# Kernel tuning notes

Hardware: AMD Instinct MI355X
Metric: run time of the kernel (lower is better)

## Reference

```python
import jax, jax.numpy as jnp
import numpy as np

EPS_NORM = 1e-12
BN_EPS = 1e-5

def rmsnorm(x, gamma):
    # F.normalize(x, dim=-1) * gamma * dim**0.5
    n = jnp.maximum(jnp.linalg.norm(x, axis=-1, keepdims=True), EPS_NORM)
    return x / n * gamma * np.float32(np.sqrt(x.shape[-1]))

def conv1d(x, w, pad):
    # x: (B,C,T), w: (O,I,K)
    return jax.lax.conv_general_dilated(x, w, (1,), [(pad, pad)],
                                        dimension_numbers=('NCH', 'OIH', 'NCH'))

def maxpool3(x):
    # kernel 3, stride 1, pad 1 over last axis
    return jax.lax.reduce_window(x, -jnp.inf, jax.lax.max,
                                 (1, 1, 3), (1, 1, 1), [(0, 0), (0, 0), (1, 1)])

def gelu(x):
    return jax.nn.gelu(x, approximate=False)  # matches torch F.gelu default


def setup_inputs() -> dict:
    key = jax.random.key(0)
    ks = jax.random.split(key, 16)
    B, N, D, E, H, NF = 4, 4096, 512, 4, 1024, 32
    s = 0.02
    inp = {
        'x': jax.random.normal(ks[0], (B, N, D), jnp.float32),
        'left_k': 2048,
        'gamma1': jnp.ones((D,), jnp.float32),
        'gamma2': jnp.ones((D,), jnp.float32),
        'attn_w': jax.random.normal(ks[1], (D, 1), jnp.float32) * s,
        'attn_b': jnp.zeros((1,), jnp.float32),
        'gate_w': jax.random.normal(ks[2], (D, E), jnp.float32) * s,
        'expert_w1': jax.random.normal(ks[3], (E, D, H), jnp.float32) * s,
        'expert_w2': jax.random.normal(ks[4], (E, H, D), jnp.float32) * s,
        'bott_w': jax.random.normal(ks[5], (NF, D, 1), jnp.float32) * s,
        'conv_w39': jax.random.normal(ks[6], (NF, NF, 39), jnp.float32) * s,
        'conv_w19': jax.random.normal(ks[7], (NF, NF, 19), jnp.float32) * s,
        'conv_w9': jax.random.normal(ks[8], (NF, NF, 9), jnp.float32) * s,
        'mp_w': jax.random.normal(ks[9], (NF, D, 1), jnp.float32) * s,
        'bn_g': jnp.ones((NF * 4,), jnp.float32),
        'bn_b': jnp.zeros((NF * 4,), jnp.float32),
        'proj_w': jax.random.normal(ks[10], (NF * 4, D), jnp.float32) * s,
        'proj_b': jnp.zeros((D,), jnp.float32),
    }
    return inp


def reference(x, left_k, gamma1, gamma2, attn_w, attn_b, gate_w,
              expert_w1, expert_w2, bott_w, conv_w39, conv_w19, conv_w9,
              mp_w, bn_g, bn_b, proj_w, proj_b):
    B, N, D = x.shape
    E = gate_w.shape[-1]

    x_n = rmsnorm(x, gamma1)
    scores = jax.nn.sigmoid(x_n @ attn_w + attn_b)            # (B,N,1)
    xs = x_n * scores                                          # (B,N,D)

    # top-k token selection (remain_ratio < 1 path)
    _, top_idx = jax.lax.top_k(scores[..., 0], left_k)         # (B,left_k)
    sorted_idx = jnp.sort(top_idx, axis=1)
    left_x = jnp.take_along_axis(xs, sorted_idx[..., None], axis=1)
    # complement sum via scatter mask (faithful to scatter_/gather/sum)
    sel = jnp.zeros((B, N), x.dtype).at[jnp.arange(B)[:, None], sorted_idx].set(1.0)
    extra = jnp.einsum('bn,bnd->bd', 1.0 - sel, xs)[:, None, :]
    xcat = jnp.concatenate([left_x, extra], axis=1)            # (B,left_k+1,D)

    x_n2 = rmsnorm(xcat, gamma2)

    # dense soft MoE
    gate = jax.nn.softmax(x_n2 @ gate_w, axis=-1)              # (B,T,E)
    h = gelu(jnp.einsum('btd,edh->bteh', x_n2, expert_w1))
    eo = jnp.einsum('bteh,ehd->bted', h, expert_w2)
    moe_out = jnp.einsum('bte,bted->btd', gate, eo)
    moe_loss = E * jnp.sum(jnp.mean(gate, axis=(0, 1)) ** 2)

    # Inception branch (channels-first)
    xc = jnp.transpose(x_n2, (0, 2, 1))                        # (B,D,T)
    xb = conv1d(xc, bott_w, 0)                                 # (B,32,T)
    outs = [conv1d(xb, conv_w39, 19), conv1d(xb, conv_w19, 9),
            conv1d(xb, conv_w9, 4), conv1d(maxpool3(xc), mp_w, 0)]
    cat = jnp.concatenate(outs, axis=1)                        # (B,128,T)
    mu = jnp.mean(cat, axis=(0, 2), keepdims=True)
    var = jnp.var(cat, axis=(0, 2), keepdims=True)
    bn = (cat - mu) / jnp.sqrt(var + BN_EPS) * bn_g[None, :, None] + bn_b[None, :, None]
    incep = gelu(bn)
    incep_out = jnp.transpose(incep, (0, 2, 1)) @ proj_w + proj_b  # (B,T,D)

    out = xcat + moe_out + incep_out
    return gelu(out), moe_loss
```

## Files before the change

### kernel.cpp

```cpp
#include <hip/hip_runtime.h>
#include <hip/hip_bf16.h>
#include <math.h>

#define DEV __device__ __forceinline__

constexpr int B_ = 4, N_ = 4096, D_ = 512, E_ = 4, H_ = 1024, NF_ = 32;
constexpr int KL_ = 2048, T_ = KL_ + 1;
constexpr int TOK_ = B_ * T_;
constexpr int SP_ = 2304;

typedef __bf16 bf16x8 __attribute__((ext_vector_type(8)));
typedef float f32x4 __attribute__((ext_vector_type(4)));

DEV float gelu_f(float x){
  float t = __expf(-1.702f * x);
  return x * __builtin_amdgcn_rcpf(1.0f + t);
}
DEV float bf2f(unsigned short u){ union{unsigned int i; float f;} c; c.i = (unsigned)u << 16; return c.f; }
DEV unsigned pack2(float a, float b){
  __hip_bfloat16 ha = __float2bfloat16(a), hb = __float2bfloat16(b);
  unsigned short ua = *(unsigned short*)&ha, ub = *(unsigned short*)&hb;
  return (unsigned)ua | ((unsigned)ub << 16);
}

DEV float wave_sum(float v){
  #pragma unroll
  for (int off = 32; off > 0; off >>= 1) v += __shfl_down(v, off, 64);
  return v;
}

DEV float block_sum256(float v, float* sm){
  v = wave_sum(v);
  int lane = threadIdx.x & 63, wid = threadIdx.x >> 6;
  if (lane == 0) sm[wid] = v;
  __syncthreads();
  if (threadIdx.x == 0) sm[0] = sm[0] + sm[1] + sm[2] + sm[3];
  __syncthreads();
  float r = sm[0];
  __syncthreads();
  return r;
}

__global__ void k_rms_score(const float* __restrict__ x, const float* __restrict__ g,
                            const float* __restrict__ aw, const float* __restrict__ ab,
                            float* __restrict__ scores, float* __restrict__ scale){
  __shared__ float sm[4];
  int row = blockIdx.x; int tid = threadIdx.x;
  const float* xr = x + (size_t)row * D_;
  float v0 = xr[tid], v1 = xr[tid + 256];
  float ss = block_sum256(v0 * v0 + v1 * v1, sm);
  float a  = block_sum256(v0 * g[tid] * aw[tid] + v1 * g[tid + 256] * aw[tid + 256], sm);
  float n = fmaxf(sqrtf(ss), 1e-12f);
  float inv = 22.627416997969522f / n;
  float z = inv * a + ab[0];
  float s = 1.0f / (1.0f + expf(-z));
  if (tid == 0){ scores[row] = s; scale[row] = inv * s; }
}

__global__ void k_select(const float* __restrict__ scores, int* __restrict__ flags){
  __shared__ float s[N_];
  __shared__ int cnts[4][64];
  int b = blockIdx.y; int tid = threadIdx.x;
  int tile = blockIdx.x * 64;
  const float4* src = (const float4*)(scores + (size_t)b * N_);
  for (int j = tid; j < N_ / 4; j += 256) ((float4*)s)[j] = src[j];
  __syncthreads();
  int tok = tid & 63, part = tid >> 6;
  int i = tile + tok;
  float si = s[i];
  int cnt = 0;
  const float4* sp = (const float4*)(s + part * 1024);
  int jb = part * 1024;
  #pragma unroll 4
  for (int j = 0; j < 256; j++){
    float4 v = sp[j];
    int j4 = jb + j * 4;
    cnt += (v.x > si) || (v.x == si && (j4 + 0) < i);
    cnt += (v.y > si) || (v.y == si && (j4 + 1) < i);
    cnt += (v.z > si) || (v.z == si && (j4 + 2) < i);
    cnt += (v.w > si) || (v.w == si && (j4 + 3) < i);
  }
  cnts[part][tok] = cnt;
  __syncthreads();
  if (tid < 64){
    int c = cnts[0][tid] + cnts[1][tid] + cnts[2][tid] + cnts[3][tid];
    flags[(size_t)b * N_ + tile + tid] = (c < KL_) ? 1 : 0;
  }
}

__global__ void k_compact(const int* __restrict__ flags, int* __restrict__ idx){
  __shared__ int wsum[4];
  int b = blockIdx.x; int tid = threadIdx.x;
  const int* fb = flags + (size_t)b * N_;
  int f[16]; int cnt = 0;
  #pragma unroll
  for (int i = 0; i < 16; i++){ f[i] = fb[tid * 16 + i]; cnt += f[i]; }
  int lane = tid & 63, wid = tid >> 6;
  int v = cnt;
  #pragma unroll
  for (int off = 1; off < 64; off <<= 1){
    int t = __shfl_up(v, off, 64);
    if (lane >= off) v += t;
  }
  if (lane == 63) wsum[wid] = v;
  __syncthreads();
  int base = v - cnt;
  for (int w = 0; w < wid; w++) base += wsum[w];
  int* ib = idx + (size_t)b * KL_;
  #pragma unroll
  for (int i = 0; i < 16; i++){
    if (f[i]) ib[base++] = tid * 16 + i;
  }
}

DEV void rms2_tail(int row, float xc0, float xc1,
                   const float* __restrict__ g2, const float* __restrict__ gw,
                   __hip_bfloat16* __restrict__ xcatb,
                   __hip_bfloat16* __restrict__ xn2b, float* __restrict__ gate,
                   float* sm, float* sg){
  int tid = threadIdx.x;
  __hip_bfloat16* xb = xcatb + (size_t)row * D_;
  xb[tid] = __float2bfloat16(xc0); xb[tid + 256] = __float2bfloat16(xc1);
  float ss = block_sum256(xc0 * xc0 + xc1 * xc1, sm);
  float n = fmaxf(sqrtf(ss), 1e-12f);
  float inv = 22.627416997969522f / n;
  float xn0 = xc0 * inv * g2[tid], xn1 = xc1 * inv * g2[tid + 256];
  __hip_bfloat16* ob = xn2b + (size_t)row * D_;
  ob[tid] = __float2bfloat16(xn0); ob[tid + 256] = __float2bfloat16(xn1);
  const float4* gw4 = (const float4*)gw;
  float4 wa = gw4[tid], wb = gw4[tid + 256];
  float l0 = xn0 * wa.x + xn1 * wb.x, l1 = xn0 * wa.y + xn1 * wb.y;
  float l2 = xn0 * wa.z + xn1 * wb.z, l3 = xn0 * wa.w + xn1 * wb.w;
  l0 = wave_sum(l0); l1 = wave_sum(l1); l2 = wave_sum(l2); l3 = wave_sum(l3);
  int lane = tid & 63, wid = tid >> 6;
  if (lane == 0){ sg[wid*4+0]=l0; sg[wid*4+1]=l1; sg[wid*4+2]=l2; sg[wid*4+3]=l3; }
  __syncthreads();
  if (tid == 0){
    float a0 = sg[0]+sg[4]+sg[8]+sg[12];
    float a1 = sg[1]+sg[5]+sg[9]+sg[13];
    float a2 = sg[2]+sg[6]+sg[10]+sg[14];
    float a3 = sg[3]+sg[7]+sg[11]+sg[15];
    float m = fmaxf(fmaxf(a0, a1), fmaxf(a2, a3));
    float e0 = expf(a0-m), e1 = expf(a1-m), e2 = expf(a2-m), e3 = expf(a3-m);
    float is = 1.f / (e0+e1+e2+e3);
    float* gr = gate + (size_t)row * 4;
    gr[0]=e0*is; gr[1]=e1*is; gr[2]=e2*is; gr[3]=e3*is;
  }
}

__global__ void k_gatherrms(const float* __restrict__ x, const float* __restrict__ scale,
                            const float* __restrict__ g1, const float* __restrict__ g2,
                            const float* __restrict__ gw, const int* __restrict__ idx,
                            __hip_bfloat16* __restrict__ xcatb,
                            __hip_bfloat16* __restrict__ xn2b, float* __restrict__ gate){
  __shared__ float sm[4];
  __shared__ float sg[16];
  int rid = blockIdx.x;
  int b = rid >> 11, p = rid & (KL_ - 1);
  int tid = threadIdx.x;
  int tok = idx[(size_t)b * KL_ + p];
  float sc = scale[(size_t)b * N_ + tok];
  const float* xr = x + ((size_t)b * N_ + tok) * D_;
  float xc0 = xr[tid] * sc * g1[tid];
  float xc1 = xr[tid + 256] * sc * g1[tid + 256];
  rms2_tail(b * T_ + p, xc0, xc1, g2, gw, xcatb, xn2b, gate, sm, sg);
}

__global__ void k_extra1(const float* __restrict__ x, const float* __restrict__ scale,
                         const int* __restrict__ flags, float* __restrict__ part){
  int b = blockIdx.y, blk = blockIdx.x;
  int tid = threadIdx.x;
  const int* fb = flags + (size_t)b * N_ + blk * 64;
  const float* sb = scale + (size_t)b * N_ + blk * 64;
  const float2* xp = (const float2*)(x + ((size_t)b * N_ + blk * 64) * D_) + tid;
  float2 acc = {0.f, 0.f};
  for (int i = 0; i < 64; i++){
    if (!fb[i]){
      float s = sb[i];
      float2 v = xp[(size_t)i * 256];
      acc.x += v.x * s; acc.y += v.y * s;
    }
  }
  float* pr = part + ((size_t)(b * 64 + blk)) * D_;
  pr[tid * 2] = acc.x; pr[tid * 2 + 1] = acc.y;
}

__global__ void k_extra2r(const float* __restrict__ part, const float* __restrict__ g1,
                          const float* __restrict__ g2, const float* __restrict__ gw,
                          __hip_bfloat16* __restrict__ xcatb,
                          __hip_bfloat16* __restrict__ xn2b, float* __restrict__ gate){
  __shared__ float sm[4];
  __shared__ float sg[16];
  int b = blockIdx.x; int tid = threadIdx.x;
  float s0 = 0.f, s1 = 0.f;
  for (int i = 0; i < 64; i++){
    const float* pr = part + ((size_t)(b * 64 + i)) * D_;
    s0 += pr[tid]; s1 += pr[tid + 256];
  }
  float xc0 = s0 * g1[tid], xc1 = s1 * g1[tid + 256];
  rms2_tail(b * T_ + KL_, xc0, xc1, g2, gw, xcatb, xn2b, gate, sm, sg);
}

__global__ void k_gsumloss(const float* __restrict__ gate, float* __restrict__ o){
  __shared__ float sm[16];
  int tid = threadIdx.x;
  float4 a = {0.f, 0.f, 0.f, 0.f};
  for (int r = tid; r < TOK_; r += 256){
    float4 v = *(const float4*)(gate + (size_t)r * 4);
    a.x += v.x; a.y += v.y; a.z += v.z; a.w += v.w;
  }
  a.x = wave_sum(a.x); a.y = wave_sum(a.y); a.z = wave_sum(a.z); a.w = wave_sum(a.w);
  int lane = tid & 63, wid = tid >> 6;
  if (lane == 0){ sm[wid*4]=a.x; sm[wid*4+1]=a.y; sm[wid*4+2]=a.z; sm[wid*4+3]=a.w; }
  __syncthreads();
  if (tid == 0){
    float l = 0.f;
    #pragma unroll
    for (int e = 0; e < 4; e++){
      float s = sm[e] + sm[4+e] + sm[8+e] + sm[12+e];
      float m = s / (float)TOK_;
      l += m * m;
    }
    o[0] = (float)E_ * l;
  }
}

DEV void trb_tile(const float* __restrict__ in, __hip_bfloat16* __restrict__ out,
                  int R, int C, int bx, int by){
  __shared__ float t[32][33];
  int c0 = bx * 32, r0 = by * 32;
  int j = threadIdx.x & 31, i4 = threadIdx.x >> 5;
  #pragma unroll
  for (int k = 0; k < 4; k++){
    int i = i4 * 4 + k;
    t[i][j] = in[(size_t)(r0 + i) * C + c0 + j];
  }
  __syncthreads();
  #pragma unroll
  for (int k = 0; k < 4; k++){
    int i = i4 * 4 + k;
    out[(size_t)(c0 + i) * R + r0 + j] = __float2bfloat16(t[j][i]);
  }
}

__global__ void k_wprep(const float* __restrict__ ew1, const float* __restrict__ ew2,
                        const float* __restrict__ proj_w,
                        const float* __restrict__ w39, const float* __restrict__ w19,
                        const float* __restrict__ w9,
                        __hip_bfloat16* __restrict__ w1b, __hip_bfloat16* __restrict__ w2b,
                        __hip_bfloat16* __restrict__ projb, __hip_bfloat16* __restrict__ wcb,
                        float* __restrict__ stats){
  int blk = blockIdx.x;
  int tid = threadIdx.x;
  if (blk < 2048){
    int e = blk >> 9, rem = blk & 511;
    int by = rem >> 5, bx = rem & 31;
    trb_tile(ew1 + (size_t)e * D_ * H_, w1b + (size_t)e * D_ * H_, D_, H_, bx, by);
  } else if (blk < 4096){
    int r = blk - 2048;
    int e = r >> 9, r2 = r & 511;
    int bx = r2 & 15, by = r2 >> 4;
    __shared__ float t[32][33];
    const float* ip = ew2 + (size_t)e * H_ * D_;
    __hip_bfloat16* op = w2b + (size_t)e * H_;
    int c0 = bx * 32, r0 = by * 32;
    int j = tid & 31, i4 = tid >> 5;
    #pragma unroll
    for (int k = 0; k < 4; k++){
      int i = i4 * 4 + k;
      t[i][j] = ip[(size_t)(r0 + i) * D_ + c0 + j];
    }
    __syncthreads();
    #pragma unroll
    for (int k = 0; k < 4; k++){
      int i = i4 * 4 + k;
      int v = r0 + j;
      int pv = (v & ~63) | ((v & 15) << 2) | ((v >> 4) & 3);
      op[(size_t)(c0 + i) * 4096 + pv] = __float2bfloat16(t[j][i]);
    }
  } else if (blk < 4160){
    int r = blk - 4096;
    trb_tile(proj_w, projb, 128, D_, r & 15, r >> 4);
  } else if (blk < 4448){
    int i = (blk - 4160) * 256 + tid;
    if (i < 73728){
      const float* w; int KP, KW, base;
      if (i < 40960){ w = w39; KP = 40; KW = 39; base = 0; }
      else if (i < 61440){ w = w19; KP = 20; KW = 19; base = 40960; }
      else { w = w9; KP = 12; KW = 9; base = 61440; }
      int li = i - base;
      int oc = li / (32 * KP);
      int rem = li % (32 * KP);
      int k = rem >> 5, ic = rem & 31;
      float v = (k < KW) ? w[((size_t)oc * 32 + ic) * KW + k] : 0.f;
      wcb[i] = __float2bfloat16(v);
    }
  } else {
    stats[tid] = 0.f;
  }
}

template<int EPI>
__launch_bounds__(512)
__global__ void gemm_bt(const __hip_bfloat16* __restrict__ A,
                        const __hip_bfloat16* __restrict__ Bt,
                        __hip_bfloat16* __restrict__ Cb, size_t zstride,
                        int M, int N, int K, int kloc,
                        const float* __restrict__ gatep){
  __shared__ __align__(16) char smem[2][24576];
  int tid = threadIdx.x;
  unsigned gx = gridDim.x;
  unsigned nwg = gx * gridDim.y;
  unsigned orig = blockIdx.x + gx * blockIdx.y;
  unsigned q = nwg >> 3, r = nwg & 7;
  unsigned xcd = orig & 7, loc = orig >> 3;
  unsigned wg = (xcd < r ? xcd * (q + 1) : r * (q + 1) + (xcd - r) * q) + loc;
  int m0 = (int)(wg / gx) * 256, n0 = (int)(wg % gx) * 128;
  int z = blockIdx.z;
  int koff = z * kloc;
  int ln = tid & 63, wid = tid >> 6;
  int wm = wid >> 1, wn = wid & 1;

  f32x4 acc[4][4] = {};

  auto stage = [&](int buf, int k0){
    #pragma unroll
    for (int c = 0; c < 2; c++){
      int ii = tid + c * 512;
      int rr = ii >> 2, s = ii & 3;
      int gm = m0 + rr; gm = gm < M ? gm : M - 1;
      const __hip_bfloat16* gp = A + (size_t)gm * K + (koff + k0 + ((s ^ (rr & 3)) << 3));
      __builtin_amdgcn_global_load_lds(
          (const __attribute__((address_space(1))) void*)gp,
          (__attribute__((address_space(3))) void*)&smem[buf][ii * 16], 16, 0, 0);
    }
    {
      int ii = tid;
      int rr = ii >> 2, s = ii & 3;
      const __hip_bfloat16* gp = Bt + (size_t)(n0 + rr) * K + (koff + k0 + ((s ^ (rr & 3)) << 3));
      __builtin_amdgcn_global_load_lds(
          (const __attribute__((address_space(1))) void*)gp,
          (__attribute__((address_space(3))) void*)&smem[buf][16384 + ii * 16], 16, 0, 0);
    }
  };

  int nk = kloc >> 5;
  stage(0, 0);
  __syncthreads();
  int slotb = (((ln >> 4) ^ (ln & 3)) << 4);
  for (int t = 0; t < nk; t++){
    int buf = t & 1;
    if (t + 1 < nk) stage(buf ^ 1, (t + 1) << 5);
    bf16x8 af[4], bfr[4];
    #pragma unroll
    for (int m = 0; m < 4; m++){
      int R = wm * 64 + m * 16 + (ln & 15);
      af[m] = *(const bf16x8*)&smem[buf][R * 64 + slotb];
    }
    #pragma unroll
    for (int n = 0; n < 4; n++){
      int R = wn * 64 + n * 16 + (ln & 15);
      bfr[n] = *(const bf16x8*)&smem[buf][16384 + R * 64 + slotb];
    }
    #pragma unroll
    for (int m = 0; m < 4; m++)
      #pragma unroll
      for (int n = 0; n < 4; n++)
        acc[m][n] = __builtin_amdgcn_mfma_f32_16x16x32_bf16(af[m], bfr[n], acc[m][n], 0, 0, 0);
    __syncthreads();
  }

  __hip_bfloat16* Co = Cb + (size_t)z * zstride;
  int e = n0 >> 10;
  int lr = ln & 15;
  #pragma unroll
  for (int m = 0; m < 4; m++){
    int rb = m0 + wm * 64 + m * 16 + ((ln >> 4) << 2);
    float gv[4];
    if (EPI == 1){
      #pragma unroll
      for (int r2 = 0; r2 < 4; r2++)
        gv[r2] = (rb + r2 < M) ? gatep[(size_t)(rb + r2) * 4 + e] : 0.f;
    }
    #pragma unroll
    for (int r2 = 0; r2 < 4; r2++){
      int row = rb + r2;
      if (row < M){
        float v0 = acc[m][0][r2], v1 = acc[m][1][r2];
        float v2 = acc[m][2][r2], v3 = acc[m][3][r2];
        if (EPI == 1){
          v0 = gelu_f(v0) * gv[r2]; v1 = gelu_f(v1) * gv[r2];
          v2 = gelu_f(v2) * gv[r2]; v3 = gelu_f(v3) * gv[r2];
        }
        uint2 pk; pk.x = pack2(v0, v1); pk.y = pack2(v2, v3);
        size_t ci = (size_t)row * N + (n0 + wn * 64 + 4 * lr);
        *(uint2*)&Co[ci] = pk;
      }
    }
  }
}

__global__ void k_1x1F(const __hip_bfloat16* __restrict__ xn2b, const float* __restrict__ bw,
                       const float* __restrict__ mw,
                       __hip_bfloat16* __restrict__ xbp, float* __restrict__ cat,
                       float* __restrict__ stats){
  __shared__ float Xs[32 * 33];
  __shared__ float Ws[32 * 36];
  int type = blockIdx.y;
  const float* w = type == 0 ? bw : mw;
  int tid = threadIdx.x;
  int G0 = blockIdx.x * 32;
  int tok = tid & 31, grp = tid >> 5;
  float acc[4] = {};
  for (int d0 = 0; d0 < D_; d0 += 32){
    {
      int tt = tid >> 3, dc = (tid & 7) * 4;
      int g = G0 + tt;
      float4 v = {0.f, 0.f, 0.f, 0.f};
      if (g < TOK_){
        const __hip_bfloat16* p = xn2b + (size_t)g * D_ + d0 + dc;
        ushort4 rw = *(const ushort4*)p;
        v.x = bf2f(rw.x); v.y = bf2f(rw.y); v.z = bf2f(rw.z); v.w = bf2f(rw.w);
        if (type == 1){
          int t = g % T_;
          if (t > 0){
            ushort4 u = *(const ushort4*)(p - D_);
            v.x = fmaxf(v.x, bf2f(u.x)); v.y = fmaxf(v.y, bf2f(u.y));
            v.z = fmaxf(v.z, bf2f(u.z)); v.w = fmaxf(v.w, bf2f(u.w));
          }
          if (t < T_ - 1){
            ushort4 u = *(const ushort4*)(p + D_);
            v.x = fmaxf(v.x, bf2f(u.x)); v.y = fmaxf(v.y, bf2f(u.y));
            v.z = fmaxf(v.z, bf2f(u.z)); v.w = fmaxf(v.w, bf2f(u.w));
          }
        }
      }
      float* xd = &Xs[tt * 33 + dc];
      xd[0] = v.x; xd[1] = v.y; xd[2] = v.z; xd[3] = v.w;
    }
    for (int j = tid; j < 1024; j += 256){
      int f = j >> 5, d = j & 31;
      Ws[d * 36 + f] = w[(size_t)f * D_ + d0 + d];
    }
    __syncthreads();
    const float* xr = &Xs[tok * 33];
    #pragma unroll 8
    for (int d = 0; d < 32; d++){
      float xv = xr[d];
      const float4* w4 = (const float4*)&Ws[d * 36 + grp * 4];
      float4 a = w4[0];
      acc[0] += xv * a.x; acc[1] += xv * a.y; acc[2] += xv * a.z; acc[3] += xv * a.w;
    }
    __syncthreads();
  }
  int g = G0 + tok;
  bool valid = g < TOK_;
  if (valid){
    if (type == 0){
      int bb = g / T_, t = g % T_;
      __hip_bfloat16* op = xbp + ((size_t)(bb * SP_ + 32 + t)) * 32 + grp * 4;
      #pragma unroll
      for (int j = 0; j < 4; j++) op[j] = __float2bfloat16(acc[j]);
    } else {
      float* op = cat + (size_t)g * 128 + 96 + grp * 4;
      #pragma unroll
      for (int j = 0; j < 4; j++) op[j] = acc[j];
    }
  }
  if (type == 1){
    #pragma unroll
    for (int j = 0; j < 4; j++){
      float s = valid ? acc[j] : 0.f;
      float qv = valid ? acc[j] * acc[j] : 0.f;
      #pragma unroll
      for (int off = 16; off > 0; off >>= 1){
        s += __shfl_down(s, off, 32);
        qv += __shfl_down(qv, off, 32);
      }
      if (tok == 0){
        int ch = 96 + grp * 4 + j;
        atomicAdd(&stats[ch], s);
        atomicAdd(&stats[128 + ch], qv);
      }
    }
  }
}

template<int KP, int PAD, int OFF, int TYPE>
DEV void convm_body(const __hip_bfloat16* __restrict__ xbp,
                    const __hip_bfloat16* __restrict__ wcb,
                    float* __restrict__ cat, float* __restrict__ stats,
                    char* smem, float* bsS, float* bsQ){
  constexpr int R = KP * 32;
  int t0 = blockIdx.x * 128, b = blockIdx.y;
  int tid = threadIdx.x;
  if (tid < 32){ bsS[tid] = 0.f; bsQ[tid] = 0.f; }
  for (int j = tid; j < 768; j += 256){
    int r = j >> 2, c = j & 3;
    int rg = b * SP_ + 32 + t0 - PAD + r;
    const __hip_bfloat16* gp = xbp + (size_t)rg * 32 + ((c ^ (r & 3)) << 3);
    __builtin_amdgcn_global_load_lds(
        (const __attribute__((address_space(1))) void*)gp,
        (__attribute__((address_space(3))) void*)(smem + j * 16), 16, 0, 0);
  }
  __syncthreads();
  int ln = tid & 63, wid = tid >> 6;
  int lr = ln & 15, lg = ln >> 4;
  int tb = wid * 32;
  const __hip_bfloat16* wt = wcb + OFF;
  const __hip_bfloat16* bp0 = wt + (size_t)lr * R + lg * 8;
  const __hip_bfloat16* bp1 = wt + (size_t)(16 + lr) * R + lg * 8;
  f32x4 acc[2][2] = {};
  bf16x8 bc0 = *(const bf16x8*)bp0;
  bf16x8 bc1 = *(const bf16x8*)bp1;
  #pragma unroll 4
  for (int s = 0; s < KP; s++){
    bf16x8 bn0 = bc0, bn1 = bc1;
    if (s + 1 < KP){
      bn0 = *(const bf16x8*)(bp0 + (s + 1) * 32);
      bn1 = *(const bf16x8*)(bp1 + (s + 1) * 32);
    }
    int ra0 = tb + lr + s;
    int ra1 = tb + 16 + lr + s;
    bf16x8 a0 = *(const bf16x8*)(smem + ra0 * 64 + ((lg ^ (ra0 & 3)) << 4));
    bf16x8 a1 = *(const bf16x8*)(smem + ra1 * 64 + ((lg ^ (ra1 & 3)) << 4));
    acc[0][0] = __builtin_amdgcn_mfma_f32_16x16x32_bf16(a0, bc0, acc[0][0], 0, 0, 0);
    acc[0][1] = __builtin_amdgcn_mfma_f32_16x16x32_bf16(a0, bc1, acc[0][1], 0, 0, 0);
    acc[1][0] = __builtin_amdgcn_mfma_f32_16x16x32_bf16(a1, bc0, acc[1][0], 0, 0, 0);
    acc[1][1] = __builtin_amdgcn_mfma_f32_16x16x32_bf16(a1, bc1, acc[1][1], 0, 0, 0);
    bc0 = bn0; bc1 = bn1;
  }
  float sN[2] = {0.f, 0.f}, qN[2] = {0.f, 0.f};
  #pragma unroll
  for (int m = 0; m < 2; m++){
    int rb = tb + m * 16 + (lg << 2);
    #pragma unroll
    for (int n = 0; n < 2; n++){
      int oc = n * 16 + lr;
      #pragma unroll
      for (int j2 = 0; j2 < 4; j2++){
        int tp = t0 + rb + j2;
        if (tp < T_){
          float v = acc[m][n][j2];
          cat[((size_t)b * T_ + tp) * 128 + TYPE * 32 + oc] = v;
          sN[n] += v; qN[n] += v * v;
        }
      }
    }
  }
  #pragma unroll
  for (int n = 0; n < 2; n++){
    float s = sN[n], qv = qN[n];
    s += __shfl_down(s, 32, 64); qv += __shfl_down(qv, 32, 64);
    s += __shfl_down(s, 16, 64); qv += __shfl_down(qv, 16, 64);
    if (ln < 16){
      atomicAdd(&bsS[n * 16 + lr], s);
      atomicAdd(&bsQ[n * 16 + lr], qv);
    }
  }
  __syncthreads();
  if (tid < 32){
    atomicAdd(&stats[TYPE * 32 + tid], bsS[tid]);
    atomicAdd(&stats[128 + TYPE * 32 + tid], bsQ[tid]);
  }
}

__global__ __launch_bounds__(256)
void k_convM(const __hip_bfloat16* __restrict__ xbp,
             const __hip_bfloat16* __restrict__ wcb, float* __restrict__ cat,
             float* __restrict__ stats){
  __shared__ __align__(16) char smem[192 * 64];
  __shared__ float bsS[32], bsQ[32];
  if (blockIdx.z == 0)      convm_body<40, 19, 0,     0>(xbp, wcb, cat, stats, smem, bsS, bsQ);
  else if (blockIdx.z == 1) convm_body<20, 9,  40960, 1>(xbp, wcb, cat, stats, smem, bsS, bsQ);
  else                      convm_body<12, 4,  61440, 2>(xbp, wcb, cat, stats, smem, bsS, bsQ);
}

__global__ void k_bnact(const float* __restrict__ cat, __hip_bfloat16* __restrict__ catb,
                        const float* __restrict__ stats,
                        const float* __restrict__ g, const float* __restrict__ b){
  int i = blockIdx.x * 256 + threadIdx.x;
  int c = i & 127;
  float mu = stats[c] * (1.f / TOK_);
  float var = stats[128 + c] * (1.f / TOK_) - mu * mu;
  float v = cat[i];
  v = (v - mu) * rsqrtf(var + 1e-5f) * g[c] + b[c];
  catb[i] = __float2bfloat16(gelu_f(v));
}

__global__ void k_final(const __hip_bfloat16* __restrict__ xcatb,
                        const __hip_bfloat16* __restrict__ moeb,
                        size_t zs, const __hip_bfloat16* __restrict__ ioutb,
                        const float* __restrict__ pb, float* __restrict__ out){
  size_t i = ((size_t)blockIdx.x * 256 + threadIdx.x) * 2;
  int p = (int)(i & 511);
  size_t rowbase = i - p;
  float s0 = 0.f, s1 = 0.f;
  #pragma unroll
  for (int z = 0; z < 4; z++){
    unsigned u = *(const unsigned*)&moeb[(size_t)z * zs + i];
    s0 += bf2f((unsigned short)(u & 0xffff));
    s1 += bf2f((unsigned short)(u >> 16));
  }
  unsigned v = *(const unsigned*)&ioutb[i];
  s0 += bf2f((unsigned short)(v & 0xffff));
  s1 += bf2f((unsigned short)(v >> 16));
  int d0 = (p & ~63) | ((p & 3) << 4) | ((p >> 2) & 15);
  int p1 = p + 1;
  int d1 = (p1 & ~63) | ((p1 & 3) << 4) | ((p1 >> 2) & 15);
  const unsigned short* xc = (const unsigned short*)xcatb;
  s0 += bf2f(xc[rowbase + d0]) + pb[d0];
  s1 += bf2f(xc[rowbase + d1]) + pb[d1];
  out[rowbase + d0] = gelu_f(s0);
  out[rowbase + d1] = gelu_f(s1);
}

extern "C" void kernel_launch(void* const* d_in, const int* in_sizes, int n_in,
                              void* d_out, int out_size, void* d_ws, size_t ws_size,
                              hipStream_t stream){
  const float* x      = (const float*)d_in[0];
  const float* gamma1 = (const float*)d_in[2];
  const float* gamma2 = (const float*)d_in[3];
  const float* attn_w = (const float*)d_in[4];
  const float* attn_b = (const float*)d_in[5];
  const float* gate_w = (const float*)d_in[6];
  const float* ew1    = (const float*)d_in[7];
  const float* ew2    = (const float*)d_in[8];
  const float* bott_w = (const float*)d_in[9];
  const float* w39    = (const float*)d_in[10];
  const float* w19    = (const float*)d_in[11];
  const float* w9     = (const float*)d_in[12];
  const float* mp_w   = (const float*)d_in[13];
  const float* bn_g   = (const float*)d_in[14];
  const float* bn_b   = (const float*)d_in[15];
  const float* proj_w = (const float*)d_in[16];
  const float* proj_b = (const float*)d_in[17];
  float* out = (float*)d_out;

  float* ws = (float*)d_ws;
  size_t off = 0;
  auto alloc = [&](size_t n){ size_t o = off; off += (n + 63) & ~(size_t)63; return o; };
  size_t f_hb   = alloc((size_t)TOK_ * 4096 / 2);
  size_t f_sc   = alloc(B_ * N_);
  size_t f_sca  = alloc(B_ * N_);
  size_t f_fl   = alloc(B_ * N_);
  size_t f_idx  = alloc(B_ * KL_);
  size_t f_xcb  = alloc((size_t)TOK_ * D_ / 2 + 64);
  size_t f_moeb = alloc((size_t)4 * TOK_ * D_ / 2 + 64);
  size_t f_gate = alloc(TOK_ * E_);
  size_t f_st   = alloc(256);
  size_t f_xbp  = alloc((size_t)B_ * SP_ * 32 / 2);
  size_t f_cat  = alloc((size_t)TOK_ * 128);
  size_t f_wb   = alloc((size_t)(E_ * D_ * H_) + (size_t)TOK_ * D_ / 2 + 64);
  size_t f_part = alloc((size_t)B_ * 64 * D_);
  size_t f_wcb  = alloc(73728 / 2 + 64);
  size_t f_pjb  = alloc(512 * 128 / 2 + 64);
  (void)ws_size; (void)in_sizes; (void)n_in; (void)out_size;

  float* sc   = ws + f_sc;
  float* sca  = ws + f_sca;
  int*   fl   = (int*)(ws + f_fl);
  int*   idx  = (int*)(ws + f_idx);
  float* gate = ws + f_gate;
  float* stats= ws + f_st;
  float* cat  = ws + f_cat;
  float* part = ws + f_part;
  __hip_bfloat16* xcatb = (__hip_bfloat16*)(ws + f_xcb);
  __hip_bfloat16* moeb  = (__hip_bfloat16*)(ws + f_moeb);
  __hip_bfloat16* xbp   = (__hip_bfloat16*)(ws + f_xbp);
  __hip_bfloat16* wcb   = (__hip_bfloat16*)(ws + f_wcb);
  __hip_bfloat16* projb = (__hip_bfloat16*)(ws + f_pjb);
  __hip_bfloat16* hbuf  = (__hip_bfloat16*)(ws + f_hb);
  __hip_bfloat16* ioutb = (__hip_bfloat16*)(ws + f_hb);
  __hip_bfloat16* catb  = (__hip_bfloat16*)(ws + f_hb + 4196416);
  __hip_bfloat16* w1b  = (__hip_bfloat16*)(ws + f_wb);
  __hip_bfloat16* w2b  = w1b + (size_t)E_ * D_ * H_;
  __hip_bfloat16* xn2b = w2b + (size_t)E_ * D_ * H_;

  hipMemsetAsync(xbp, 0, (size_t)B_ * SP_ * 32 * sizeof(__hip_bfloat16), stream);

  k_wprep<<<4449, 256, 0, stream>>>(ew1, ew2, proj_w, w39, w19, w9,
                                    w1b, w2b, projb, wcb, stats);

  k_rms_score<<<B_ * N_, 256, 0, stream>>>(x, gamma1, attn_w, attn_b, sc, sca);
  k_select<<<dim3(N_ / 64, B_), 256, 0, stream>>>(sc, fl);
  k_compact<<<B_, 256, 0, stream>>>(fl, idx);
  k_gatherrms<<<B_ * KL_, 256, 0, stream>>>(x, sca, gamma1, gamma2, gate_w, idx,
                                            xcatb, xn2b, gate);
  k_extra1<<<dim3(64, B_), 256, 0, stream>>>(x, sca, fl, part);
  k_extra2r<<<B_, 256, 0, stream>>>(part, gamma1, gamma2, gate_w, xcatb, xn2b, gate);
  k_gsumloss<<<1, 256, 0, stream>>>(gate, out + (size_t)TOK_ * D_);

  int mt = (TOK_ + 255) / 256;
  size_t zs = (size_t)TOK_ * D_;
  gemm_bt<1><<<dim3(4096/128, mt), 512, 0, stream>>>(
      xn2b, w1b, hbuf, 0, TOK_, 4096, D_, D_, gate);
  gemm_bt<0><<<dim3(D_/128, mt, 4), 512, 0, stream>>>(
      hbuf, w2b, moeb, zs, TOK_, D_, 4096, 1024, nullptr);

  int t32 = (TOK_ + 31) / 32;
  k_1x1F<<<dim3(t32, 2), 256, 0, stream>>>(xn2b, bott_w, mp_w, xbp, cat, stats);
  k_convM<<<dim3(17, 4, 3), 256, 0, stream>>>(xbp, wcb, cat, stats);
  k_bnact<<<(TOK_ * 128) / 256, 256, 0, stream>>>(cat, catb, stats, bn_g, bn_b);
  gemm_bt<0><<<dim3(D_/128, mt), 512, 0, stream>>>(
      catb, projb, ioutb, 0, TOK_, D_, 128, 128, nullptr);
  k_final<<<((size_t)TOK_ * D_) / 512, 256, 0, stream>>>(xcatb, moeb, zs, ioutb, proj_b, out);
}
```

Before: 317.3 us.

## Move BatchNorm statistics out of conv kernels into a dedicated reduction pass

Removes the per-block shuffle/atomic accumulation of BatchNorm sum and sum-of-squares from the 1x1 and multi-kernel conv kernels and adds a separate k_bnstat kernel that rereads the cat buffer to compute per-channel statistics. It also doubles the reduction tile in k_1x1F from 32 to 64 channels per iteration, halving the sync count. The intent is to cut atomic contention and epilogue work in the conv kernels, at the cost of an extra kernel launch and an additional full read of the cat buffer.

New measurement: 297.3 us. 6.3% less time.

```diff
diff --git a/kernel.cpp b/kernel.cpp
--- a/kernel.cpp
+++ b/kernel.cpp
@@ -402,19 +402,19 @@
 
 __global__ void k_1x1F(const __hip_bfloat16* __restrict__ xn2b, const float* __restrict__ bw,
                        const float* __restrict__ mw,
-                       __hip_bfloat16* __restrict__ xbp, float* __restrict__ cat,
-                       float* __restrict__ stats){
-  __shared__ float Xs[32 * 33];
-  __shared__ float Ws[32 * 36];
+                       __hip_bfloat16* __restrict__ xbp, float* __restrict__ cat){
+  __shared__ float Xs[32 * 65];
+  __shared__ float Ws[64 * 36];
   int type = blockIdx.y;
   const float* w = type == 0 ? bw : mw;
   int tid = threadIdx.x;
   int G0 = blockIdx.x * 32;
   int tok = tid & 31, grp = tid >> 5;
   float acc[4] = {};
-  for (int d0 = 0; d0 < D_; d0 += 32){
-    {
-      int tt = tid >> 3, dc = (tid & 7) * 4;
+  for (int d0 = 0; d0 < D_; d0 += 64){
+    #pragma unroll
+    for (int j = tid; j < 512; j += 256){
+      int tt = j >> 4, dc = (j & 15) * 4;
       int g = G0 + tt;
       float4 v = {0.f, 0.f, 0.f, 0.f};
       if (g < TOK_){
@@ -435,17 +435,18 @@
           }
         }
       }
-      float* xd = &Xs[tt * 33 + dc];
+      float* xd = &Xs[tt * 65 + dc];
       xd[0] = v.x; xd[1] = v.y; xd[2] = v.z; xd[3] = v.w;
     }
-    for (int j = tid; j < 1024; j += 256){
-      int f = j >> 5, d = j & 31;
+    #pragma unroll
+    for (int j = tid; j < 2048; j += 256){
+      int f = j >> 6, d = j & 63;
       Ws[d * 36 + f] = w[(size_t)f * D_ + d0 + d];
     }
     __syncthreads();
-    const float* xr = &Xs[tok * 33];
+    const float* xr = &Xs[tok * 65];
     #pragma unroll 8
-    for (int d = 0; d < 32; d++){
+    for (int d = 0; d < 64; d++){
       float xv = xr[d];
       const float4* w4 = (const float4*)&Ws[d * 36 + grp * 4];
       float4 a = w4[0];
@@ -454,8 +455,7 @@
     __syncthreads();
   }
   int g = G0 + tok;
-  bool valid = g < TOK_;
-  if (valid){
+  if (g < TOK_){
     if (type == 0){
       int bb = g / T_, t = g % T_;
       __hip_bfloat16* op = xbp + ((size_t)(bb * SP_ + 32 + t)) * 32 + grp * 4;
@@ -467,34 +467,15 @@
       for (int j = 0; j < 4; j++) op[j] = acc[j];
     }
   }
-  if (type == 1){
-    #pragma unroll
-    for (int j = 0; j < 4; j++){
-      float s = valid ? acc[j] : 0.f;
-      float qv = valid ? acc[j] * acc[j] : 0.f;
-      #pragma unroll
-      for (int off = 16; off > 0; off >>= 1){
-        s += __shfl_down(s, off, 32);
-        qv += __shfl_down(qv, off, 32);
-      }
-      if (tok == 0){
-        int ch = 96 + grp * 4 + j;
-        atomicAdd(&stats[ch], s);
-        atomicAdd(&stats[128 + ch], qv);
-      }
-    }
-  }
 }
 
 template<int KP, int PAD, int OFF, int TYPE>
 DEV void convm_body(const __hip_bfloat16* __restrict__ xbp,
                     const __hip_bfloat16* __restrict__ wcb,
-                    float* __restrict__ cat, float* __restrict__ stats,
-                    char* smem, float* bsS, float* bsQ){
+                    float* __restrict__ cat, char* smem){
   constexpr int R = KP * 32;
   int t0 = blockIdx.x * 128, b = blockIdx.y;
   int tid = threadIdx.x;
-  if (tid < 32){ bsS[tid] = 0.f; bsQ[tid] = 0.f; }
   for (int j = tid; j < 768; j += 256){
     int r = j >> 2, c = j & 3;
     int rg = b * SP_ + 32 + t0 - PAD + r;
@@ -530,7 +511,6 @@
     acc[1][1] = __builtin_amdgcn_mfma_f32_16x16x32_bf16(a1, bc1, acc[1][1], 0, 0, 0);
     bc0 = bn0; bc1 = bn1;
   }
-  float sN[2] = {0.f, 0.f}, qN[2] = {0.f, 0.f};
   #pragma unroll
   for (int m = 0; m < 2; m++){
     int rb = tb + m * 16 + (lg << 2);
@@ -540,40 +520,36 @@
       #pragma unroll
       for (int j2 = 0; j2 < 4; j2++){
         int tp = t0 + rb + j2;
-        if (tp < T_){
-          float v = acc[m][n][j2];
-          cat[((size_t)b * T_ + tp) * 128 + TYPE * 32 + oc] = v;
-          sN[n] += v; qN[n] += v * v;
-        }
+        if (tp < T_)
+          cat[((size_t)b * T_ + tp) * 128 + TYPE * 32 + oc] = acc[m][n][j2];
       }
     }
-  }
-  #pragma unroll
-  for (int n = 0; n < 2; n++){
-    float s = sN[n], qv = qN[n];
-    s += __shfl_down(s, 32, 64); qv += __shfl_down(qv, 32, 64);
-    s += __shfl_down(s, 16, 64); qv += __shfl_down(qv, 16, 64);
-    if (ln < 16){
-      atomicAdd(&bsS[n * 16 + lr], s);
-      atomicAdd(&bsQ[n * 16 + lr], qv);
-    }
-  }
-  __syncthreads();
-  if (tid < 32){
-    atomicAdd(&stats[TYPE * 32 + tid], bsS[tid]);
-    atomicAdd(&stats[128 + TYPE * 32 + tid], bsQ[tid]);
   }
 }
 
 __global__ __launch_bounds__(256)
 void k_convM(const __hip_bfloat16* __restrict__ xbp,
-             const __hip_bfloat16* __restrict__ wcb, float* __restrict__ cat,
-             float* __restrict__ stats){
+             const __hip_bfloat16* __restrict__ wcb, float* __restrict__ cat){
   __shared__ __align__(16) char smem[192 * 64];
-  __shared__ float bsS[32], bsQ[32];
-  if (blockIdx.z == 0)      convm_body<40, 19, 0,     0>(xbp, wcb, cat, stats, smem, bsS, bsQ);
-  else if (blockIdx.z == 1) convm_body<20, 9,  40960, 1>(xbp, wcb, cat, stats, smem, bsS, bsQ);
-  else                      convm_body<12, 4,  61440, 2>(xbp, wcb, cat, stats, smem, bsS, bsQ);
+  if (blockIdx.z == 0)      convm_body<40, 19, 0,     0>(xbp, wcb, cat, smem);
+  else if (blockIdx.z == 1) convm_body<20, 9,  40960, 1>(xbp, wcb, cat, smem);
+  else                      convm_body<12, 4,  61440, 2>(xbp, wcb, cat, smem);
+}
+
+__global__ void k_bnstat(const float* __restrict__ cat, float* __restrict__ stats){
+  __shared__ float sm[512];
+  int tid = threadIdx.x;
+  float s = 0.f, q = 0.f;
+  for (int rp = blockIdx.x; rp < TOK_ / 2; rp += gridDim.x){
+    float v = cat[(size_t)rp * 256 + tid];
+    s += v; q += v * v;
+  }
+  sm[tid] = s; sm[256 + tid] = q;
+  __syncthreads();
+  if (tid < 128){
+    atomicAdd(&stats[tid], sm[tid] + sm[tid + 128]);
+    atomicAdd(&stats[128 + tid], sm[256 + tid] + sm[256 + tid + 128]);
+  }
 }
 
 __global__ void k_bnact(const float* __restrict__ cat, __hip_bfloat16* __restrict__ catb,
@@ -699,8 +675,9 @@
       hbuf, w2b, moeb, zs, TOK_, D_, 4096, 1024, nullptr);
 
   int t32 = (TOK_ + 31) / 32;
-  k_1x1F<<<dim3(t32, 2), 256, 0, stream>>>(xn2b, bott_w, mp_w, xbp, cat, stats);
-  k_convM<<<dim3(17, 4, 3), 256, 0, stream>>>(xbp, wcb, cat, stats);
+  k_1x1F<<<dim3(t32, 2), 256, 0, stream>>>(xn2b, bott_w, mp_w, xbp, cat);
+  k_convM<<<dim3(17, 4, 3), 256, 0, stream>>>(xbp, wcb, cat);
+  k_bnstat<<<256, 256, 0, stream>>>(cat, stats);
   k_bnact<<<(TOK_ * 128) / 256, 256, 0, stream>>>(cat, catb, stats, bn_g, bn_b);
   gemm_bt<0><<<dim3(D_/128, mt), 512, 0, stream>>>(
       catb, projb, ioutb, 0, TOK_, D_, 128, 128, nullptr);
```
